# Optimization experiments

Hardware: AMD Instinct MI355X
Metric: run time of the kernel (lower is better)

## Reference

```python
import jax, jax.numpy as jnp
import numpy as np

IGNORE_INDEX = -100

def setup_inputs() -> dict:
    key = jax.random.key(0)
    k1, k2, k3 = jax.random.split(key, 3)
    N, H, V = 2048, 2048, 128256
    x = jax.random.normal(k1, (N, H), dtype=jnp.float32)
    weight = jax.random.normal(k2, (H, V), dtype=jnp.float32) * 0.02
    labels = jax.random.randint(k3, (N,), 0, V, dtype=jnp.int32)
    return {"x": x, "weight": weight, "labels": labels}

def reference(x, weight, labels):
    # logits computed in float32, matching kernel's float accumulation
    logits = jnp.matmul(x, weight).astype(jnp.float32)  # [N, V]
    lse = jax.scipy.special.logsumexp(logits, axis=-1)  # [N]
    tgt_idx = jnp.clip(labels, 0, logits.shape[-1] - 1)
    target_logits = jnp.take_along_axis(logits, tgt_idx[:, None], axis=-1)[:, 0]
    valid = (labels != IGNORE_INDEX).astype(jnp.float32)
    loss = (lse - target_logits) * valid  # per-token loss, zeroed at ignore_index
    return loss, lse
```

## Files before the change

### kernel.cpp

```cpp
#include <hip/hip_runtime.h>

#define V_DIM 128256
#define K_DIM 2048
#define M_DIM 2048
#define NPB (V_DIM / 256)
#define NS (K_DIM / 128)

using f32x4  = __attribute__((ext_vector_type(4))) float;
using i32x4  = __attribute__((ext_vector_type(4))) int;

#define QX_MAX 5.2f
#define QW_MAX 0.125f
#define SCF ((QX_MAX / 127.f) * (QW_MAX / 127.f))

static __device__ __forceinline__ signed char q8(float v, float s) {
  int q = __float2int_rn(v * s);
  q = q < -127 ? -127 : (q > 127 ? 127 : q);
  return (signed char)q;
}

__global__ __launch_bounds__(256) void quant_x(const float* __restrict__ x,
                                               signed char* __restrict__ xq) {
  const size_t i = ((size_t)blockIdx.x * 256 + threadIdx.x) * 8;
  const float4 a = *(const float4*)&x[i];
  const float4 b = *(const float4*)&x[i + 4];
  const float s = 127.f / QX_MAX;
  union { signed char c[8]; int2 v; } o;
  o.c[0] = q8(a.x, s); o.c[1] = q8(a.y, s); o.c[2] = q8(a.z, s); o.c[3] = q8(a.w, s);
  o.c[4] = q8(b.x, s); o.c[5] = q8(b.y, s); o.c[6] = q8(b.z, s); o.c[7] = q8(b.w, s);
  *(int2*)&xq[i] = o.v;
}

__global__ __launch_bounds__(256) void transpose_w(const float* __restrict__ wgt,
                                                   signed char* __restrict__ wtc,
                                                   int c0) {
  __shared__ signed char tile[64][68];
  const int t  = threadIdx.x;
  const int cb = blockIdx.x * 64;
  const int kb = blockIdx.y * 64;
  const int tc4 = (t & 15) * 4;
  const int tk  = t >> 4;
  const float s = 127.f / QW_MAX;
#pragma unroll
  for (int p = 0; p < 4; ++p) {
    const int k = kb + tk + p * 16;
    const float4 v = *(const float4*)&wgt[(size_t)k * V_DIM + (c0 + cb + tc4)];
    tile[tc4 + 0][tk + p * 16] = q8(v.x, s);
    tile[tc4 + 1][tk + p * 16] = q8(v.y, s);
    tile[tc4 + 2][tk + p * 16] = q8(v.z, s);
    tile[tc4 + 3][tk + p * 16] = q8(v.w, s);
  }
  __syncthreads();
  const int wk4 = (t & 15) * 4;
  const int wc  = t >> 4;
#pragma unroll
  for (int p = 0; p < 4; ++p) {
    const int c = wc + p * 16;
    uchar4 o;
    o.x = (unsigned char)tile[c][wk4 + 0];
    o.y = (unsigned char)tile[c][wk4 + 1];
    o.z = (unsigned char)tile[c][wk4 + 2];
    o.w = (unsigned char)tile[c][wk4 + 3];
    *(uchar4*)&wtc[(size_t)(cb + c) * K_DIM + (kb + wk4)] = o;
  }
}

#define MF(a, b, c) __builtin_amdgcn_mfma_i32_16x16x64_i8(a, b, c, 0, 0, 0)

#define STAGE_A(T, q, d) do {                                                   \
    const int rb_ = 32 * (q) + (w & 3) * 8 + (w >> 2) * 128;                    \
    __builtin_amdgcn_global_load_lds(                                           \
        (const __attribute__((address_space(1))) void*)                         \
            &xq[(size_t)(m0 + rb_ + lr) * K_DIM + (T) * 128 + sw16],            \
        (__attribute__((address_space(3))) void*)&Al[d][rb_ * 128], 16, 0, 0);  \
  } while (0)

#define STAGE_B(T, i, d) do {                                                   \
    const int rb_ = (i) * 64 + w * 8;                                           \
    __builtin_amdgcn_global_load_lds(                                           \
        (const __attribute__((address_space(1))) void*)                         \
            &wt[(size_t)(n0 + rb_ + lr) * K_DIM + (T) * 128 + sw16],            \
        (__attribute__((address_space(3))) void*)&Bl[d][rb_ * 128], 16, 0, 0);  \
  } while (0)

#define RD_A(c, mi, s) (*(const i32x4*)&Al[c][(wm * 128 + (mi) * 16 + (l & 15)) * 128 + \
                                              ((((s) * 4 + (l >> 4)) ^ (l & 7)) * 16)])
#define RD_B(c, ni, s) (*(const i32x4*)&Bl[c][(wn * 64 + (ni) * 16 + (l & 15)) * 128 + \
                                              ((((s) * 4 + (l >> 4)) ^ (l & 7)) * 16)])

#define MFMA8(mi, aa0, aa1)                                        \
  acc[mi][0] = MF(aa0, bfr[0][0], acc[mi][0]);                     \
  acc[mi][0] = MF(aa1, bfr[0][1], acc[mi][0]);                     \
  acc[mi][1] = MF(aa0, bfr[1][0], acc[mi][1]);                     \
  acc[mi][1] = MF(aa1, bfr[1][1], acc[mi][1]);                     \
  acc[mi][2] = MF(aa0, bfr[2][0], acc[mi][2]);                     \
  acc[mi][2] = MF(aa1, bfr[2][1], acc[mi][2]);                     \
  acc[mi][3] = MF(aa0, bfr[3][0], acc[mi][3]);                     \
  acc[mi][3] = MF(aa1, bfr[3][1], acc[mi][3]);

__global__ __launch_bounds__(512, 2) void gemm_lse(const signed char* __restrict__ xq,
                                                   const signed char* __restrict__ wt,
                                                   const int* __restrict__ labels,
                                                   float* __restrict__ partial,
                                                   float* __restrict__ tgt,
                                                   int c0, int nbx) {
  __shared__ signed char Al[2][256 * 128];
  __shared__ signed char Bl[2][256 * 128];
  __shared__ int larr[256];

  const int tid = threadIdx.x;
  const int w = tid >> 6, l = tid & 63;
  const int wm = w >> 2, wn = w & 3;

  const int nwg = nbx * 8;
  const int swz = (blockIdx.x & 7) * (nwg >> 3) + (blockIdx.x >> 3);
  const int m0 = (swz & 7) * 256;
  const int n0 = (swz >> 3) * 256;
  const int gn0 = c0 + n0;

  const int lr = l >> 3;
  const int sw16 = ((l & 7) ^ lr) * 16;

  i32x4 acc[8][4] = {};
  i32x4 bfr[4][2];

  if (tid < 256) larr[tid] = labels[m0 + tid];

  STAGE_A(0, 0, 0); STAGE_B(0, 0, 0); STAGE_A(0, 1, 0); STAGE_B(0, 1, 0);
  STAGE_A(0, 2, 0); STAGE_B(0, 2, 0); STAGE_A(0, 3, 0); STAGE_B(0, 3, 0);
  STAGE_A(1, 0, 1); STAGE_B(1, 0, 1);
  STAGE_A(1, 1, 1); STAGE_B(1, 1, 1);
  asm volatile("s_waitcnt vmcnt(4)" ::: "memory");
  __builtin_amdgcn_s_barrier();

#pragma unroll 1
  for (int t = 0; t < NS; ++t) {
    const int cb = t & 1;
    {
      bfr[0][0] = RD_B(cb, 0, 0); bfr[1][0] = RD_B(cb, 1, 0);
      bfr[2][0] = RD_B(cb, 2, 0); bfr[3][0] = RD_B(cb, 3, 0);
      bfr[0][1] = RD_B(cb, 0, 1); bfr[1][1] = RD_B(cb, 1, 1);
      bfr[2][1] = RD_B(cb, 2, 1); bfr[3][1] = RD_B(cb, 3, 1);
      i32x4 a00 = RD_A(cb, 0, 0), a01 = RD_A(cb, 0, 1);
      i32x4 a10 = RD_A(cb, 1, 0), a11 = RD_A(cb, 1, 1);
      i32x4 a20 = RD_A(cb, 2, 0), a21 = RD_A(cb, 2, 1);
      i32x4 a30 = RD_A(cb, 3, 0), a31 = RD_A(cb, 3, 1);
      if (t + 1 < NS) {
        STAGE_A(t + 1, 2, cb ^ 1); STAGE_B(t + 1, 2, cb ^ 1);
        STAGE_A(t + 1, 3, cb ^ 1); STAGE_B(t + 1, 3, cb ^ 1);
      }
      __builtin_amdgcn_s_setprio(1);
      MFMA8(0, a00, a01);
      MFMA8(1, a10, a11);
      MFMA8(2, a20, a21);
      MFMA8(3, a30, a31);
      __builtin_amdgcn_s_setprio(0);
      __builtin_amdgcn_s_barrier();
    }
    {
      i32x4 a40 = RD_A(cb, 4, 0), a41 = RD_A(cb, 4, 1);
      i32x4 a50 = RD_A(cb, 5, 0), a51 = RD_A(cb, 5, 1);
      i32x4 a60 = RD_A(cb, 6, 0), a61 = RD_A(cb, 6, 1);
      i32x4 a70 = RD_A(cb, 7, 0), a71 = RD_A(cb, 7, 1);
      if (t + 2 < NS) {
        STAGE_A(t + 2, 0, cb); STAGE_B(t + 2, 0, cb);
        STAGE_A(t + 2, 1, cb); STAGE_B(t + 2, 1, cb);
      }
      __builtin_amdgcn_s_setprio(1);
      MFMA8(4, a40, a41);
      MFMA8(5, a50, a51);
      MFMA8(6, a60, a61);
      MFMA8(7, a70, a71);
      __builtin_amdgcn_s_setprio(0);
      if (t + 2 < NS) asm volatile("s_waitcnt vmcnt(4)" ::: "memory");
      else            asm volatile("s_waitcnt vmcnt(0)" ::: "memory");
      __builtin_amdgcn_s_barrier();
    }
  }

  {
    const int colbase = wn * 64 + (l & 15);
#pragma unroll
    for (int mi = 0; mi < 8; ++mi)
#pragma unroll
      for (int r = 0; r < 4; ++r) {
        const int row = wm * 128 + mi * 16 + (l >> 4) * 4 + r;
        int lab = larr[row];
        lab = lab < 0 ? 0 : (lab >= V_DIM ? V_DIM - 1 : lab);
        const int cl = lab - gn0;
#pragma unroll
        for (int ni = 0; ni < 4; ++ni)
          if (cl == colbase + ni * 16) tgt[m0 + row] = (float)acc[mi][ni][r] * SCF;
      }
  }

  const float e2 = SCF * 1.4426950408889634f;
  float rs[8][4];
#pragma unroll
  for (int mi = 0; mi < 8; ++mi)
#pragma unroll
    for (int r = 0; r < 4; ++r) {
      float s = 0.f;
#pragma unroll
      for (int ni = 0; ni < 4; ++ni)
        s += exp2f((float)acc[mi][ni][r] * e2);
#pragma unroll
      for (int off = 1; off <= 8; off <<= 1) s += __shfl_xor(s, off, 64);
      rs[mi][r] = s;
    }
  __syncthreads();
  float* red = (float*)&Al[0][0];
  if ((l & 15) == 0) {
#pragma unroll
    for (int mi = 0; mi < 8; ++mi)
#pragma unroll
      for (int r = 0; r < 4; ++r)
        red[wn * 256 + wm * 128 + mi * 16 + (l >> 4) * 4 + r] = rs[mi][r];
  }
  __syncthreads();
  if (tid < 256) {
    const float tot = (red[tid] + red[256 + tid]) + (red[512 + tid] + red[768 + tid]);
    partial[(size_t)(m0 + tid) * NPB + (c0 / 256 + (swz >> 3))] = tot;
  }
}

__global__ __launch_bounds__(256) void reduce_lse(const float* __restrict__ partial,
                                                  const float* __restrict__ tgt,
                                                  const int* __restrict__ labels,
                                                  float* __restrict__ out) {
  const int row = blockIdx.x;
  float s = 0.f;
  for (int vb = threadIdx.x; vb < NPB; vb += 256)
    s += partial[(size_t)row * NPB + vb];
#pragma unroll
  for (int off = 1; off < 64; off <<= 1) s += __shfl_xor(s, off, 64);
  __shared__ float w4[4];
  if ((threadIdx.x & 63) == 0) w4[threadIdx.x >> 6] = s;
  __syncthreads();
  if (threadIdx.x == 0) {
    const float tot = (w4[0] + w4[1]) + (w4[2] + w4[3]);
    const float lse = logf(tot);
    const float loss = (labels[row] != -100) ? (lse - tgt[row]) : 0.f;
    out[row] = loss;
    out[M_DIM + row] = lse;
  }
}

extern "C" void kernel_launch(void* const* d_in, const int* in_sizes, int n_in,
                              void* d_out, int out_size, void* d_ws, size_t ws_size,
                              hipStream_t stream) {
  const float* x = (const float*)d_in[0];
  const float* wgt = (const float*)d_in[1];
  const int* labels = (const int*)d_in[2];
  float* out = (float*)d_out;

  char* ws = (char*)d_ws;
  signed char* xq = (signed char*)ws;
  size_t off = (size_t)M_DIM * K_DIM;
  float* partial = (float*)(ws + off);
  off += (size_t)M_DIM * NPB * 4;
  float* tgt = (float*)(ws + off);
  off += (size_t)M_DIM * 4;
  off = (off + 255) & ~(size_t)255;
  signed char* wtc = (signed char*)(ws + off);
  const size_t avail = ws_size > off ? ws_size - off : 0;
  int CC = 16384;
  while (CC > 256 && (size_t)CC * K_DIM > avail) CC >>= 1;

  quant_x<<<dim3(M_DIM * K_DIM / (256 * 8)), dim3(256), 0, stream>>>(x, xq);
  for (int c0 = 0; c0 < V_DIM; c0 += CC) {
    int cc = V_DIM - c0;
    if (cc > CC) cc = CC;
    transpose_w<<<dim3(cc / 64, K_DIM / 64), dim3(256), 0, stream>>>(wgt, wtc, c0);
    const int nbx = cc / 256;
    gemm_lse<<<dim3(nbx * 8), dim3(512), 0, stream>>>(xq, wtc, labels, partial, tgt,
                                                      c0, nbx);
  }
  reduce_lse<<<dim3(M_DIM), dim3(256), 0, stream>>>(partial, tgt, labels, out);
}
```

Measured before the change: 844.7 us.

## Fuse next-chunk weight quantize-transpose into GEMM epilogue with double buffering

The weight quantize-transpose for the next vocab chunk now runs inside the GEMM kernel's epilogue, writing into a second ping-pong buffer, so only the first chunk needs a standalone transpose launch. The standalone transpose is rewritten without shared memory: each thread reads 16 strided floats down one column and writes 16 contiguous int8s. The aim is to remove separate launches and let transpose memory traffic overlap with MFMA work from other blocks. The cost is column-strided global reads, extra epilogue time in every GEMM block, and a fixed workspace requirement of two chunk buffers with no fallback when the workspace is smaller.

```diff
diff --git a/kernel.cpp b/kernel.cpp
--- a/kernel.cpp
+++ b/kernel.cpp
@@ -5,6 +5,7 @@
 #define M_DIM 2048
 #define NPB (V_DIM / 256)
 #define NS (K_DIM / 128)
+#define CC 16384
 
 using f32x4  = __attribute__((ext_vector_type(4))) float;
 using i32x4  = __attribute__((ext_vector_type(4))) int;
@@ -34,34 +35,20 @@
 __global__ __launch_bounds__(256) void transpose_w(const float* __restrict__ wgt,
                                                    signed char* __restrict__ wtc,
                                                    int c0) {
-  __shared__ signed char tile[64][68];
-  const int t  = threadIdx.x;
-  const int cb = blockIdx.x * 64;
-  const int kb = blockIdx.y * 64;
-  const int tc4 = (t & 15) * 4;
-  const int tk  = t >> 4;
+  const int col = blockIdx.x * 64 + (threadIdx.x & 63);
+  const int kb0 = blockIdx.y * 512 + (threadIdx.x >> 6) * 128;
   const float s = 127.f / QW_MAX;
-#pragma unroll
-  for (int p = 0; p < 4; ++p) {
-    const int k = kb + tk + p * 16;
-    const float4 v = *(const float4*)&wgt[(size_t)k * V_DIM + (c0 + cb + tc4)];
-    tile[tc4 + 0][tk + p * 16] = q8(v.x, s);
-    tile[tc4 + 1][tk + p * 16] = q8(v.y, s);
-    tile[tc4 + 2][tk + p * 16] = q8(v.z, s);
-    tile[tc4 + 3][tk + p * 16] = q8(v.w, s);
-  }
-  __syncthreads();
-  const int wk4 = (t & 15) * 4;
-  const int wc  = t >> 4;
-#pragma unroll
-  for (int p = 0; p < 4; ++p) {
-    const int c = wc + p * 16;
-    uchar4 o;
-    o.x = (unsigned char)tile[c][wk4 + 0];
-    o.y = (unsigned char)tile[c][wk4 + 1];
-    o.z = (unsigned char)tile[c][wk4 + 2];
-    o.w = (unsigned char)tile[c][wk4 + 3];
-    *(uchar4*)&wtc[(size_t)(cb + c) * K_DIM + (kb + wk4)] = o;
+#pragma unroll 1
+  for (int it = 0; it < 8; ++it) {
+    const int kb = kb0 + it * 16;
+    float v[16];
+#pragma unroll
+    for (int j = 0; j < 16; ++j)
+      v[j] = wgt[(size_t)(kb + j) * V_DIM + (c0 + col)];
+    union { signed char c[16]; uint4 u; } o;
+#pragma unroll
+    for (int j = 0; j < 16; ++j) o.c[j] = q8(v[j], s);
+    *(uint4*)&wtc[(size_t)col * K_DIM + kb] = o.u;
   }
 }
 
@@ -100,10 +87,13 @@
 
 __global__ __launch_bounds__(512, 2) void gemm_lse(const signed char* __restrict__ xq,
                                                    const signed char* __restrict__ wt,
+                                                   const float* __restrict__ wgt,
+                                                   signed char* __restrict__ wtn,
                                                    const int* __restrict__ labels,
                                                    float* __restrict__ partial,
                                                    float* __restrict__ tgt,
-                                                   int c0, int nbx) {
+                                                   int c0, int nbx,
+                                                   int c0n, int ccn) {
   __shared__ signed char Al[2][256 * 128];
   __shared__ signed char Bl[2][256 * 128];
   __shared__ int larr[256];
@@ -222,6 +212,29 @@
     const float tot = (red[tid] + red[256 + tid]) + (red[512 + tid] + red[768 + tid]);
     partial[(size_t)(m0 + tid) * NPB + (c0 / 256 + (swz >> 3))] = tot;
   }
+
+  if (c0n >= 0) {
+    const int ncb = (ccn + nwg - 1) / nwg;
+    const int colb = blockIdx.x * ncb;
+    const int cl = tid & 31;
+    if (cl < ncb && colb + cl < ccn) {
+      const int col = colb + cl;
+      const int kb0 = (tid >> 5) * 128;
+      const float s = 127.f / QW_MAX;
+#pragma unroll 1
+      for (int it = 0; it < 8; ++it) {
+        const int kb = kb0 + it * 16;
+        float v[16];
+#pragma unroll
+        for (int j = 0; j < 16; ++j)
+          v[j] = wgt[(size_t)(kb + j) * V_DIM + (c0n + col)];
+        union { signed char c[16]; uint4 u; } o;
+#pragma unroll
+        for (int j = 0; j < 16; ++j) o.c[j] = q8(v[j], s);
+        *(uint4*)&wtn[(size_t)col * K_DIM + kb] = o.u;
+      }
+    }
+  }
 }
 
 __global__ __launch_bounds__(256) void reduce_lse(const float* __restrict__ partial,
@@ -262,19 +275,23 @@
   float* tgt = (float*)(ws + off);
   off += (size_t)M_DIM * 4;
   off = (off + 255) & ~(size_t)255;
-  signed char* wtc = (signed char*)(ws + off);
-  const size_t avail = ws_size > off ? ws_size - off : 0;
-  int CC = 16384;
-  while (CC > 256 && (size_t)CC * K_DIM > avail) CC >>= 1;
+  signed char* wtc0 = (signed char*)(ws + off);
+  signed char* wtc1 = wtc0 + (size_t)CC * K_DIM;
+  signed char* wtc[2] = {wtc0, wtc1};
 
   quant_x<<<dim3(M_DIM * K_DIM / (256 * 8)), dim3(256), 0, stream>>>(x, xq);
-  for (int c0 = 0; c0 < V_DIM; c0 += CC) {
+  transpose_w<<<dim3(CC / 64, K_DIM / 512), dim3(256), 0, stream>>>(wgt, wtc[0], 0);
+  for (int c0 = 0, i = 0; c0 < V_DIM; c0 += CC, ++i) {
     int cc = V_DIM - c0;
     if (cc > CC) cc = CC;
-    transpose_w<<<dim3(cc / 64, K_DIM / 64), dim3(256), 0, stream>>>(wgt, wtc, c0);
     const int nbx = cc / 256;
-    gemm_lse<<<dim3(nbx * 8), dim3(512), 0, stream>>>(xq, wtc, labels, partial, tgt,
-                                                      c0, nbx);
+    const int c0n_raw = c0 + CC;
+    const int c0n = (c0n_raw < V_DIM) ? c0n_raw : -1;
+    int ccn = (c0n >= 0) ? (V_DIM - c0n) : 0;
+    if (ccn > CC) ccn = CC;
+    gemm_lse<<<dim3(nbx * 8), dim3(512), 0, stream>>>(
+        xq, wtc[i & 1], wgt, wtc[(i + 1) & 1], labels, partial, tgt,
+        c0, nbx, c0n, ccn);
   }
   reduce_lse<<<dim3(M_DIM), dim3(256), 0, stream>>>(partial, tgt, labels, out);
 }
```

After: 1.029 ms. 21.8% more time.
